# Optimization experiments

Hardware: AMD Instinct MI355X
Metric: run time of the kernel (lower is better)

Reference implementation:

```python
import jax, jax.numpy as jnp
import numpy as np

BETA = 0.95      # leak
THRESH = 1.0     # snntorch Leaky default threshold
ALPHA = 2.0      # ATan surrogate alpha (atan_with_alpha)
T = 100          # SPIKE_STEPS
D_IN = 65536     # input_dims
HID = 256        # fc1 hidden (hardcoded)
N_OUT = 20       # n_actions(2) * NUM_NEURONS_PER_ACTION(10)


def spike_fn(x):
    # forward of snntorch surrogate.ATan: Heaviside
    return (x > 0.0).astype(x.dtype)


def lif_step(mem, cur):
    # snntorch Leaky, reset_mechanism='subtract':
    # reset computed from previous membrane (detached), then decay+integrate, then fire
    reset = jax.lax.stop_gradient((mem > THRESH).astype(mem.dtype))
    mem_new = BETA * mem + cur - reset * THRESH
    spk = spike_fn(mem_new - THRESH)
    return spk, mem_new


def _run_net(x, W1, b1, W2, b2):
    # x: [T, D_IN]. Precompute all layer-1 currents as one big GEMM, then scan the recurrence.
    cur1_all = x @ W1.T + b1  # [T, HID]

    def step(carry, cur1):
        mem1, mem2 = carry
        spk1, mem1 = lif_step(mem1, cur1)
        cur2 = spk1 @ W2.T + b2  # [n_out]
        spk2, mem2 = lif_step(mem2, cur2)
        return (mem1, mem2), spk2

    init = (jnp.zeros((W1.shape[0],), x.dtype), jnp.zeros((W2.shape[0],), x.dtype))
    (_, mem2_final), spk2_hist = jax.lax.scan(step, init, cur1_all)
    return spk2_hist, mem2_final  # [T, n_out], [n_out]


def setup_inputs() -> dict:
    key = jax.random.key(0)
    ks = jax.random.split(key, 5)
    s = 0.01
    return {
        "poisson_spikes": jax.random.uniform(ks[0], (T, 1, D_IN), dtype=jnp.float32),
        "aW1": jax.random.normal(ks[1], (HID, D_IN), dtype=jnp.float32) * s,
        "ab1": jnp.zeros((HID,), jnp.float32),
        "aW2": jax.random.normal(ks[2], (N_OUT, HID), dtype=jnp.float32) * s,
        "ab2": jnp.zeros((N_OUT,), jnp.float32),
        "cW1": jax.random.normal(ks[3], (HID, D_IN), dtype=jnp.float32) * s,
        "cb1": jnp.zeros((HID,), jnp.float32),
        "cW2": jax.random.normal(ks[4], (1, HID), dtype=jnp.float32) * s,
        "cb2": jnp.zeros((1,), jnp.float32),
    }


def reference(poisson_spikes, aW1, ab1, aW2, ab2, cW1, cb1, cW2, cb2):
    x = poisson_spikes[:, 0, :]  # effective batch of 1 -> [T, D_IN]
    actor_spk_hist, _ = _run_net(x, aW1, ab1, aW2, ab2)        # [T, 20]
    _, critic_mem = _run_net(x, cW1, cb1, cW2, cb2)            # [1]
    spk_sum = actor_spk_hist.sum(axis=0)                       # [20] (sum over timesteps)
    action_vals = jnp.stack([spk_sum[:10].sum(), spk_sum[10:].sum()])
    policy = jax.nn.softmax(action_vals)                       # [2]
    return policy, critic_mem
```

## Files before the change

### kernel.cpp

```cpp
#include <hip/hip_runtime.h>
#include <hip/hip_bf16.h>

#define T_STEPS 100
#define D_IN    65536
#define HID     256
#define HTOT    512
#define BETA    0.95f
#define THRESH  1.0f

typedef __bf16 bf16x8 __attribute__((ext_vector_type(8)));
typedef float  f32x16 __attribute__((ext_vector_type(16)));

__device__ __forceinline__ void gload_lds16(const void* g, void* l) {
    __builtin_amdgcn_global_load_lds(
        (const __attribute__((address_space(1))) void*)g,
        (__attribute__((address_space(3))) void*)l, 16, 0, 0);
}

__global__ __launch_bounds__(256, 2) void k_gemm1(
    const float* __restrict__ aW1,
    const float* __restrict__ cW1,
    const float* __restrict__ x,
    float* __restrict__ P,
    int nsteps)
{
    const int d    = blockIdx.x;
    const int xcd  = d & 7;
    const int sl   = d >> 3;
    const int s    = xcd * 16 + (sl & 15);
    const int ht   = sl >> 4;

    const int tid  = threadIdx.x;
    const int lane = tid & 63;
    const int l31  = lane & 31;
    const int h5   = lane >> 5;
    const int wv   = tid >> 6;
    const int wt   = (wv & 1) * 64;
    const int wh   = (wv >> 1) * 64;

    __shared__ __align__(16) char smem[2][32768];

    const float* Wbase = (ht < 2) ? (aW1 + (size_t)ht * 128 * D_IN)
                                  : (cW1 + (size_t)(ht - 2) * 128 * D_IN);

    const float* xsrc[4];
    const float* wsrc[4];
#pragma unroll
    for (int o = 0; o < 4; o++) {
        const int idx = o * 256 + tid;
        const int row = idx >> 3, g = idx & 7;
        const int xrow = (row < T_STEPS) ? row : (T_STEPS - 1);
        xsrc[o] = x     + (size_t)xrow * D_IN + (g ^ (row & 7)) * 4;
        wsrc[o] = Wbase + (size_t)row  * D_IN + (g ^ (row & 7)) * 4;
    }
    const int gk0 = s * nsteps;

    f32x16 acc00, acc01, acc10, acc11;
#pragma unroll
    for (int i = 0; i < 16; i++) {
        acc00[i] = 0.f; acc01[i] = 0.f; acc10[i] = 0.f; acc11[i] = 0.f;
    }

#define STAGE(i) do {                                                         \
    char* b_ = smem[(i) & 1];                                                 \
    const int kc_ = (gk0 + (i)) * 32;                                         \
    _Pragma("unroll")                                                         \
    for (int o = 0; o < 4; o++) {                                             \
        const int g_ = o * 256 + tid;                                         \
        gload_lds16(xsrc[o] + kc_, b_ + g_ * 16);                             \
    }                                                                         \
    _Pragma("unroll")                                                         \
    for (int o = 0; o < 4; o++) {                                             \
        const int g_ = o * 256 + tid;                                         \
        gload_lds16(wsrc[o] + kc_, b_ + 16384 + g_ * 16);                     \
    }                                                                         \
} while (0)

#define CVT8(dsth, dstm, va, vb) do {                                         \
    float f_[8] = {va.x, va.y, va.z, va.w, vb.x, vb.y, vb.z, vb.w};           \
    _Pragma("unroll")                                                         \
    for (int e = 0; e < 8; e++) {                                             \
        __bf16 h = (__bf16)f_[e];                                             \
        dsth[e] = h; dstm[e] = (__bf16)(f_[e] - (float)h);                    \
    }                                                                         \
} while (0)

#define COMPUTE(i) do {                                                       \
    const char* b_ = smem[(i) & 1];                                           \
    _Pragma("unroll")                                                         \
    for (int s16 = 0; s16 < 2; s16++) {                                       \
        const int slot_ = s16 * 2 + h5;                                       \
        const int gb    = slot_ * 2;                                          \
        const int r0 = wt + l31, r1 = r0 + 32;                                \
        const char* xr0_ = b_ + r0 * 128;                                     \
        const char* xr1_ = b_ + r1 * 128;                                     \
        float4 xa0 = *(const float4*)(xr0_ + ((gb ^ (r0 & 7)) * 16));         \
        float4 xb0 = *(const float4*)(xr0_ + (((gb + 1) ^ (r0 & 7)) * 16));   \
        float4 xa1 = *(const float4*)(xr1_ + ((gb ^ (r1 & 7)) * 16));         \
        float4 xb1 = *(const float4*)(xr1_ + (((gb + 1) ^ (r1 & 7)) * 16));   \
        bf16x8 a0h, a0m, a1h, a1m;                                            \
        CVT8(a0h, a0m, xa0, xb0);                                             \
        CVT8(a1h, a1m, xa1, xb1);                                             \
        const int hrA = wh + l31, hrB = hrA + 32;                             \
        const char* wrA_ = b_ + 16384 + hrA * 128;                            \
        const char* wrB_ = b_ + 16384 + hrB * 128;                            \
        float4 waA = *(const float4*)(wrA_ + ((gb ^ (hrA & 7)) * 16));        \
        float4 wbA = *(const float4*)(wrA_ + (((gb + 1) ^ (hrA & 7)) * 16));  \
        float4 waB = *(const float4*)(wrB_ + ((gb ^ (hrB & 7)) * 16));        \
        float4 wbB = *(const float4*)(wrB_ + (((gb + 1) ^ (hrB & 7)) * 16));  \
        bf16x8 bhA, bmA, bhB, bmB;                                            \
        CVT8(bhA, bmA, waA, wbA);                                             \
        CVT8(bhB, bmB, waB, wbB);                                             \
        acc00 = __builtin_amdgcn_mfma_f32_32x32x16_bf16(a0m, bhA, acc00, 0,0,0); \
        acc00 = __builtin_amdgcn_mfma_f32_32x32x16_bf16(a0h, bmA, acc00, 0,0,0); \
        acc00 = __builtin_amdgcn_mfma_f32_32x32x16_bf16(a0h, bhA, acc00, 0,0,0); \
        acc01 = __builtin_amdgcn_mfma_f32_32x32x16_bf16(a0m, bhB, acc01, 0,0,0); \
        acc01 = __builtin_amdgcn_mfma_f32_32x32x16_bf16(a0h, bmB, acc01, 0,0,0); \
        acc01 = __builtin_amdgcn_mfma_f32_32x32x16_bf16(a0h, bhB, acc01, 0,0,0); \
        acc10 = __builtin_amdgcn_mfma_f32_32x32x16_bf16(a1m, bhA, acc10, 0,0,0); \
        acc10 = __builtin_amdgcn_mfma_f32_32x32x16_bf16(a1h, bmA, acc10, 0,0,0); \
        acc10 = __builtin_amdgcn_mfma_f32_32x32x16_bf16(a1h, bhA, acc10, 0,0,0); \
        acc11 = __builtin_amdgcn_mfma_f32_32x32x16_bf16(a1m, bhB, acc11, 0,0,0); \
        acc11 = __builtin_amdgcn_mfma_f32_32x32x16_bf16(a1h, bmB, acc11, 0,0,0); \
        acc11 = __builtin_amdgcn_mfma_f32_32x32x16_bf16(a1h, bhB, acc11, 0,0,0); \
    }                                                                         \
} while (0)

    STAGE(0);
    STAGE(1);
    for (int i = 0; i < nsteps; i++) {
        if (i + 1 < nsteps) asm volatile("s_waitcnt vmcnt(8)" ::: "memory");
        else                asm volatile("s_waitcnt vmcnt(0)" ::: "memory");
        __builtin_amdgcn_s_barrier();
        __builtin_amdgcn_sched_barrier(0);
        COMPUTE(i);
        __builtin_amdgcn_s_barrier();
        __builtin_amdgcn_sched_barrier(0);
        if (i + 2 < nsteps) STAGE(i + 2);
    }
#undef STAGE
#undef CVT8
#undef COMPUTE

    const int rbase = 4 * h5;
    float* Pb = P + (size_t)s * T_STEPS * HTOT;
    const int hA = ht * 128 + wh + l31;
    const int hB = hA + 32;
#pragma unroll
    for (int reg = 0; reg < 16; reg++) {
        const int row = (reg & 3) + rbase + 8 * (reg >> 2);
        const int t0  = wt + row;
        const int t1  = wt + 32 + row;
        if (t0 < T_STEPS) {
            Pb[(size_t)t0 * HTOT + hA] = acc00[reg];
            Pb[(size_t)t0 * HTOT + hB] = acc01[reg];
        }
        if (t1 < T_STEPS) {
            Pb[(size_t)t1 * HTOT + hA] = acc10[reg];
            Pb[(size_t)t1 * HTOT + hB] = acc11[reg];
        }
    }
}

__global__ __launch_bounds__(256) void k_reduce(
    const float* __restrict__ P,
    const float* __restrict__ ab1, const float* __restrict__ cb1,
    float* __restrict__ cur1, float* __restrict__ wsa,
    unsigned* __restrict__ cnt, int NS)
{
    if (blockIdx.x == 0 && threadIdx.x == 0) {
        wsa[0] = 0.f; wsa[1] = 0.f; *cnt = 0u;
    }
    int g2 = blockIdx.x * 256 + threadIdx.x;
    int g  = g2 * 2;
    int h0 = g & (HTOT - 1);
    float2 sum;
    sum.x = (h0 + 0 < HID) ? ab1[h0 + 0] : cb1[h0 + 0 - HID];
    sum.y = (h0 + 1 < HID) ? ab1[h0 + 1] : cb1[h0 + 1 - HID];
    for (int ss = 0; ss < NS; ss++) {
        float2 v = *(const float2*)(P + (size_t)ss * T_STEPS * HTOT + g);
        sum.x += v.x; sum.y += v.y;
    }
    *(float2*)(cur1 + g) = sum;
}

__global__ __launch_bounds__(256) void k_gemm2(
    const float* __restrict__ cur1,
    const float* __restrict__ aW2, const float* __restrict__ ab2,
    const float* __restrict__ cW2, const float* __restrict__ cb2,
    float* __restrict__ wsa, unsigned* __restrict__ cnt,
    float* __restrict__ out)
{
    const int j   = blockIdx.x;
    const int tid = threadIdx.x;

    __shared__ float W[256];
    __shared__ unsigned long long bitsL[T_STEPS][4];
    __shared__ float c2[T_STEPS];

    const float* Wsrc = (j < 20) ? (aW2 + j * 256) : cW2;
    W[tid] = Wsrc[tid];
    const int base = (j < 20) ? 0 : 256;
    const int w    = tid >> 6;

    {
        float mem = 0.f;
        for (int tb = 0; tb < T_STEPS; tb += 10) {
            float c[10];
#pragma unroll
            for (int i = 0; i < 10; i++)
                c[i] = cur1[(size_t)(tb + i) * HTOT + base + tid];
#pragma unroll
            for (int i = 0; i < 10; i++) {
                float reset = (mem > THRESH) ? THRESH : 0.f;
                mem = BETA * mem + c[i] - reset;
                unsigned long long m = __ballot(mem > THRESH);
                if ((tid & 63) == 0) bitsL[tb + i][w] = m;
            }
        }
    }
    __syncthreads();

    if (tid < T_STEPS) {
        unsigned long long m0 = bitsL[tid][0];
        unsigned long long m1 = bitsL[tid][1];
        unsigned long long m2 = bitsL[tid][2];
        unsigned long long m3 = bitsL[tid][3];
        float acc = (j < 20) ? ab2[j] : cb2[0];
#pragma unroll
        for (int b = 0; b < 64; b++) {
            acc += ((m0 >> b) & 1ULL) ? W[b]       : 0.f;
            acc += ((m1 >> b) & 1ULL) ? W[64 + b]  : 0.f;
            acc += ((m2 >> b) & 1ULL) ? W[128 + b] : 0.f;
            acc += ((m3 >> b) & 1ULL) ? W[192 + b] : 0.f;
        }
        c2[tid] = acc;
    }
    __syncthreads();

    if (tid == 0) {
        float mem = 0.f, spk = 0.f;
        for (int t = 0; t < T_STEPS; t++) {
            float reset = (mem > THRESH) ? THRESH : 0.f;
            mem = BETA * mem + c2[t] - reset;
            spk += (mem > THRESH) ? 1.f : 0.f;
        }
        if (j < 10)       atomicAdd(&wsa[0], spk);
        else if (j < 20)  atomicAdd(&wsa[1], spk);
        else              out[2] = mem;
        __threadfence();
        unsigned done = atomicAdd(cnt, 1u);
        if (done == 20u) {
            float a0 = atomicAdd(&wsa[0], 0.f);
            float a1 = atomicAdd(&wsa[1], 0.f);
            float mx = fmaxf(a0, a1);
            float e0 = expf(a0 - mx), e1 = expf(a1 - mx);
            float inv = 1.f / (e0 + e1);
            out[0] = e0 * inv;
            out[1] = e1 * inv;
        }
    }
}

extern "C" void kernel_launch(void* const* d_in, const int* in_sizes, int n_in,
                              void* d_out, int out_size, void* d_ws, size_t ws_size,
                              hipStream_t stream) {
    const float* x   = (const float*)d_in[0];
    const float* aW1 = (const float*)d_in[1];
    const float* ab1 = (const float*)d_in[2];
    const float* aW2 = (const float*)d_in[3];
    const float* ab2 = (const float*)d_in[4];
    const float* cW1 = (const float*)d_in[5];
    const float* cb1 = (const float*)d_in[6];
    const float* cW2 = (const float*)d_in[7];
    const float* cb2 = (const float*)d_in[8];
    float* out = (float*)d_out;

    const int NS = 128;
    const int nsteps = (D_IN / NS) / 32;

    float* P    = (float*)d_ws;
    float* cur1 = P + (size_t)NS * T_STEPS * HTOT;
    float* wsa  = cur1 + T_STEPS * HTOT;
    unsigned* cnt = (unsigned*)(wsa + 2);

    k_gemm1 <<<512, 256, 0, stream>>>(aW1, cW1, x, P, nsteps);
    k_reduce<<<(T_STEPS * HTOT / 2) / 256, 256, 0, stream>>>(P, ab1, cb1, cur1, wsa, cnt, NS);
    k_gemm2 <<<21, 256, 0, stream>>>(cur1, aW2, ab2, cW2, cb2, wsa, cnt, out);
}
```

Before: 88.08 us.

## Widen GEMM1 tile to 256 hidden rows, halve K-chunk, double split-K

Each k_gemm1 block now uses 512 threads and covers all 256 hidden units of one network, so each x tile is loaded once per network instead of twice. The K chunk drops from 32 to 16 floats, and the split-K count doubles to 256 slices. The intent is to cut redundant global and LDS traffic for x and to raise per-block parallelism. In exchange, the partial buffer P and the reduce kernel's work double, and the pipeline steps get shorter.

```diff
diff --git a/kernel.cpp b/kernel.cpp
--- a/kernel.cpp
+++ b/kernel.cpp
@@ -17,7 +17,7 @@
         (__attribute__((address_space(3))) void*)l, 16, 0, 0);
 }
 
-__global__ __launch_bounds__(256, 2) void k_gemm1(
+__global__ __launch_bounds__(512, 2) void k_gemm1(
     const float* __restrict__ aW1,
     const float* __restrict__ cW1,
     const float* __restrict__ x,
@@ -27,8 +27,8 @@
     const int d    = blockIdx.x;
     const int xcd  = d & 7;
     const int sl   = d >> 3;
-    const int s    = xcd * 16 + (sl & 15);
-    const int ht   = sl >> 4;
+    const int s    = xcd * 32 + (sl & 31);
+    const int ht   = sl >> 5;
 
     const int tid  = threadIdx.x;
     const int lane = tid & 63;
@@ -38,20 +38,20 @@
     const int wt   = (wv & 1) * 64;
     const int wh   = (wv >> 1) * 64;
 
-    __shared__ __align__(16) char smem[2][32768];
-
-    const float* Wbase = (ht < 2) ? (aW1 + (size_t)ht * 128 * D_IN)
-                                  : (cW1 + (size_t)(ht - 2) * 128 * D_IN);
-
-    const float* xsrc[4];
-    const float* wsrc[4];
-#pragma unroll
-    for (int o = 0; o < 4; o++) {
-        const int idx = o * 256 + tid;
-        const int row = idx >> 3, g = idx & 7;
-        const int xrow = (row < T_STEPS) ? row : (T_STEPS - 1);
-        xsrc[o] = x     + (size_t)xrow * D_IN + (g ^ (row & 7)) * 4;
-        wsrc[o] = Wbase + (size_t)row  * D_IN + (g ^ (row & 7)) * 4;
+    __shared__ __align__(16) char smem[2][24576];
+
+    const float* Wbase = ht ? cW1 : aW1;
+
+    const int xrow_raw = tid >> 2;
+    const int xg       = tid & 3;
+    const int xrow     = (xrow_raw < T_STEPS) ? xrow_raw : (T_STEPS - 1);
+    const float* xsrc  = x + (size_t)xrow * D_IN + (xg ^ (xrow_raw & 3)) * 4;
+    const float* wsrc[2];
+#pragma unroll
+    for (int o = 0; o < 2; o++) {
+        const int idx = o * 512 + tid;
+        const int row = idx >> 2, g = idx & 3;
+        wsrc[o] = Wbase + (size_t)row * D_IN + (g ^ (row & 3)) * 4;
     }
     const int gk0 = s * nsteps;
 
@@ -63,17 +63,10 @@
 
 #define STAGE(i) do {                                                         \
     char* b_ = smem[(i) & 1];                                                 \
-    const int kc_ = (gk0 + (i)) * 32;                                         \
-    _Pragma("unroll")                                                         \
-    for (int o = 0; o < 4; o++) {                                             \
-        const int g_ = o * 256 + tid;                                         \
-        gload_lds16(xsrc[o] + kc_, b_ + g_ * 16);                             \
-    }                                                                         \
-    _Pragma("unroll")                                                         \
-    for (int o = 0; o < 4; o++) {                                             \
-        const int g_ = o * 256 + tid;                                         \
-        gload_lds16(wsrc[o] + kc_, b_ + 16384 + g_ * 16);                     \
-    }                                                                         \
+    const int kc_ = (gk0 + (i)) * 16;                                         \
+    gload_lds16(xsrc + kc_, b_ + tid * 16);                                   \
+    gload_lds16(wsrc[0] + kc_, b_ + 8192 + tid * 16);                         \
+    gload_lds16(wsrc[1] + kc_, b_ + 8192 + (512 + tid) * 16);                 \
 } while (0)
 
 #define CVT8(dsth, dstm, va, vb) do {                                         \
@@ -87,49 +80,44 @@
 
 #define COMPUTE(i) do {                                                       \
     const char* b_ = smem[(i) & 1];                                           \
-    _Pragma("unroll")                                                         \
-    for (int s16 = 0; s16 < 2; s16++) {                                       \
-        const int slot_ = s16 * 2 + h5;                                       \
-        const int gb    = slot_ * 2;                                          \
-        const int r0 = wt + l31, r1 = r0 + 32;                                \
-        const char* xr0_ = b_ + r0 * 128;                                     \
-        const char* xr1_ = b_ + r1 * 128;                                     \
-        float4 xa0 = *(const float4*)(xr0_ + ((gb ^ (r0 & 7)) * 16));         \
-        float4 xb0 = *(const float4*)(xr0_ + (((gb + 1) ^ (r0 & 7)) * 16));   \
-        float4 xa1 = *(const float4*)(xr1_ + ((gb ^ (r1 & 7)) * 16));         \
-        float4 xb1 = *(const float4*)(xr1_ + (((gb + 1) ^ (r1 & 7)) * 16));   \
-        bf16x8 a0h, a0m, a1h, a1m;                                            \
-        CVT8(a0h, a0m, xa0, xb0);                                             \
-        CVT8(a1h, a1m, xa1, xb1);                                             \
-        const int hrA = wh + l31, hrB = hrA + 32;                             \
-        const char* wrA_ = b_ + 16384 + hrA * 128;                            \
-        const char* wrB_ = b_ + 16384 + hrB * 128;                            \
-        float4 waA = *(const float4*)(wrA_ + ((gb ^ (hrA & 7)) * 16));        \
-        float4 wbA = *(const float4*)(wrA_ + (((gb + 1) ^ (hrA & 7)) * 16));  \
-        float4 waB = *(const float4*)(wrB_ + ((gb ^ (hrB & 7)) * 16));        \
-        float4 wbB = *(const float4*)(wrB_ + (((gb + 1) ^ (hrB & 7)) * 16));  \
-        bf16x8 bhA, bmA, bhB, bmB;                                            \
-        CVT8(bhA, bmA, waA, wbA);                                             \
-        CVT8(bhB, bmB, waB, wbB);                                             \
-        acc00 = __builtin_amdgcn_mfma_f32_32x32x16_bf16(a0m, bhA, acc00, 0,0,0); \
-        acc00 = __builtin_amdgcn_mfma_f32_32x32x16_bf16(a0h, bmA, acc00, 0,0,0); \
-        acc00 = __builtin_amdgcn_mfma_f32_32x32x16_bf16(a0h, bhA, acc00, 0,0,0); \
-        acc01 = __builtin_amdgcn_mfma_f32_32x32x16_bf16(a0m, bhB, acc01, 0,0,0); \
-        acc01 = __builtin_amdgcn_mfma_f32_32x32x16_bf16(a0h, bmB, acc01, 0,0,0); \
-        acc01 = __builtin_amdgcn_mfma_f32_32x32x16_bf16(a0h, bhB, acc01, 0,0,0); \
-        acc10 = __builtin_amdgcn_mfma_f32_32x32x16_bf16(a1m, bhA, acc10, 0,0,0); \
-        acc10 = __builtin_amdgcn_mfma_f32_32x32x16_bf16(a1h, bmA, acc10, 0,0,0); \
-        acc10 = __builtin_amdgcn_mfma_f32_32x32x16_bf16(a1h, bhA, acc10, 0,0,0); \
-        acc11 = __builtin_amdgcn_mfma_f32_32x32x16_bf16(a1m, bhB, acc11, 0,0,0); \
-        acc11 = __builtin_amdgcn_mfma_f32_32x32x16_bf16(a1h, bmB, acc11, 0,0,0); \
-        acc11 = __builtin_amdgcn_mfma_f32_32x32x16_bf16(a1h, bhB, acc11, 0,0,0); \
-    }                                                                         \
+    const int gb = h5 * 2;                                                    \
+                                  \
+    const int r0 = wt + l31, r1 = r0 + 32;                                    \
+    float4 xa0 = *(const float4*)(b_ + (r0 * 4 + (gb       ^ (r0 & 3))) * 16);\
+    float4 xb0 = *(const float4*)(b_ + (r0 * 4 + ((gb + 1) ^ (r0 & 3))) * 16);\
+    float4 xa1 = *(const float4*)(b_ + (r1 * 4 + (gb       ^ (r1 & 3))) * 16);\
+    float4 xb1 = *(const float4*)(b_ + (r1 * 4 + ((gb + 1) ^ (r1 & 3))) * 16);\
+    bf16x8 a0h, a0m, a1h, a1m;                                                \
+    CVT8(a0h, a0m, xa0, xb0);                                                 \
+    CVT8(a1h, a1m, xa1, xb1);                                                 \
+                            \
+    const int hA = wh + l31, hB = hA + 32;                                    \
+    const char* wl_ = b_ + 8192;                                              \
+    float4 waA = *(const float4*)(wl_ + (hA * 4 + (gb       ^ (hA & 3))) * 16);\
+    float4 wbA = *(const float4*)(wl_ + (hA * 4 + ((gb + 1) ^ (hA & 3))) * 16);\
+    float4 waB = *(const float4*)(wl_ + (hB * 4 + (gb       ^ (hB & 3))) * 16);\
+    float4 wbB = *(const float4*)(wl_ + (hB * 4 + ((gb + 1) ^ (hB & 3))) * 16);\
+    bf16x8 bhA, bmA, bhB, bmB;                                                \
+    CVT8(bhA, bmA, waA, wbA);                                                 \
+    CVT8(bhB, bmB, waB, wbB);                                                 \
+    acc00 = __builtin_amdgcn_mfma_f32_32x32x16_bf16(a0m, bhA, acc00, 0,0,0);  \
+    acc00 = __builtin_amdgcn_mfma_f32_32x32x16_bf16(a0h, bmA, acc00, 0,0,0);  \
+    acc00 = __builtin_amdgcn_mfma_f32_32x32x16_bf16(a0h, bhA, acc00, 0,0,0);  \
+    acc01 = __builtin_amdgcn_mfma_f32_32x32x16_bf16(a0m, bhB, acc01, 0,0,0);  \
+    acc01 = __builtin_amdgcn_mfma_f32_32x32x16_bf16(a0h, bmB, acc01, 0,0,0);  \
+    acc01 = __builtin_amdgcn_mfma_f32_32x32x16_bf16(a0h, bhB, acc01, 0,0,0);  \
+    acc10 = __builtin_amdgcn_mfma_f32_32x32x16_bf16(a1m, bhA, acc10, 0,0,0);  \
+    acc10 = __builtin_amdgcn_mfma_f32_32x32x16_bf16(a1h, bmA, acc10, 0,0,0);  \
+    acc10 = __builtin_amdgcn_mfma_f32_32x32x16_bf16(a1h, bhA, acc10, 0,0,0);  \
+    acc11 = __builtin_amdgcn_mfma_f32_32x32x16_bf16(a1m, bhB, acc11, 0,0,0);  \
+    acc11 = __builtin_amdgcn_mfma_f32_32x32x16_bf16(a1h, bmB, acc11, 0,0,0);  \
+    acc11 = __builtin_amdgcn_mfma_f32_32x32x16_bf16(a1h, bhB, acc11, 0,0,0);  \
 } while (0)
 
     STAGE(0);
     STAGE(1);
     for (int i = 0; i < nsteps; i++) {
-        if (i + 1 < nsteps) asm volatile("s_waitcnt vmcnt(8)" ::: "memory");
+        if (i + 1 < nsteps) asm volatile("s_waitcnt vmcnt(3)" ::: "memory");
         else                asm volatile("s_waitcnt vmcnt(0)" ::: "memory");
         __builtin_amdgcn_s_barrier();
         __builtin_amdgcn_sched_barrier(0);
@@ -144,7 +132,7 @@
 
     const int rbase = 4 * h5;
     float* Pb = P + (size_t)s * T_STEPS * HTOT;
-    const int hA = ht * 128 + wh + l31;
+    const int hA = ht * 256 + wh + l31;
     const int hB = hA + 32;
 #pragma unroll
     for (int reg = 0; reg < 16; reg++) {
@@ -276,15 +264,15 @@
     const float* cb2 = (const float*)d_in[8];
     float* out = (float*)d_out;
 
-    const int NS = 128;
-    const int nsteps = (D_IN / NS) / 32;
+    const int NS = 256;
+    const int nsteps = (D_IN / NS) / 16;
 
     float* P    = (float*)d_ws;
     float* cur1 = P + (size_t)NS * T_STEPS * HTOT;
     float* wsa  = cur1 + T_STEPS * HTOT;
     unsigned* cnt = (unsigned*)(wsa + 2);
 
-    k_gemm1 <<<512, 256, 0, stream>>>(aW1, cW1, x, P, nsteps);
+    k_gemm1 <<<512, 512, 0, stream>>>(aW1, cW1, x, P, nsteps);
     k_reduce<<<(T_STEPS * HTOT / 2) / 256, 256, 0, stream>>>(P, ab1, cb1, cur1, wsa, cnt, NS);
     k_gemm2 <<<21, 256, 0, stream>>>(cur1, aW2, ab2, cW2, cb2, wsa, cnt, out);
 }
```

New measurement: 120.4 us. +36.7%, slower.
